# Optimization experiments

Measured on AMD Instinct MI355X. Metric: run time of the kernel, lower is better.

Reference implementation:

```python
import jax, jax.numpy as jnp
import numpy as np

N_NODES = 50000
N_EDGES = 300000
N_ETYPES = 4
D = 256          # input_dim == output_dim (no zero-pad branch in GatedGraphConv)
RES = 768        # res_feature_dim
N_GRAPHS = 128
N_STEPS = 8
HID = 256        # classifier hidden dim


def setup_inputs() -> dict:
    key = jax.random.key(0)
    ks = jax.random.split(key, 12)
    s = 0.05
    return {
        "features": jax.random.normal(ks[0], (N_NODES, D + RES), jnp.float32),
        "W_e": jax.random.normal(ks[1], (N_ETYPES, D, D), jnp.float32) * s,
        "b_e": jnp.zeros((N_ETYPES, D), jnp.float32),
        "W_ih": jax.random.normal(ks[2], (D, 3 * D), jnp.float32) * s,
        "W_hh": jax.random.normal(ks[3], (D, 3 * D), jnp.float32) * s,
        "b_ih": jnp.zeros((3 * D,), jnp.float32),
        "b_hh": jnp.zeros((3 * D,), jnp.float32),
        "W1": jax.random.normal(ks[4], (D + RES, HID), jnp.float32) * s,
        "b1": jnp.zeros((HID,), jnp.float32),
        "W2": jax.random.normal(ks[5], (HID, 1), jnp.float32) * s,
        "b2": jnp.zeros((1,), jnp.float32),
        "src": jax.random.randint(ks[6], (N_EDGES,), 0, N_NODES),
        "dst": jax.random.randint(ks[7], (N_EDGES,), 0, N_NODES),
        "etypes": jax.random.randint(ks[8], (N_EDGES,), 0, N_ETYPES),
        "node2graph": jnp.sort(jax.random.randint(ks[9], (N_NODES,), 0, N_GRAPHS)),
    }


def _gru_cell(x, h, W_ih, W_hh, b_ih, b_hh):
    # PyTorch GRUCell, gate order (r, z, n)
    gi = x @ W_ih + b_ih
    gh = h @ W_hh + b_hh
    i_r, i_z, i_n = jnp.split(gi, 3, axis=-1)
    h_r, h_z, h_n = jnp.split(gh, 3, axis=-1)
    r = jax.nn.sigmoid(i_r + h_r)
    z = jax.nn.sigmoid(i_z + h_z)
    n = jnp.tanh(i_n + r * h_n)
    return (1.0 - z) * n + z * h


def reference(features, W_e, b_e, W_ih, W_hh, b_ih, b_hh, W1, b1, W2, b2,
              src, dst, etypes, node2graph):
    h = features[:, :D]          # node features fed to GGNN
    res = features[:, D:]        # mixed residual features (bypass GGNN)

    def step(h, _):
        # per-edge-type linear on all nodes: [T, N, D]
        ht = jnp.einsum('nd,tde->tne', h, W_e) + b_e[:, None, :]
        msgs = ht[etypes, src]                                   # [E, D]
        a = jax.ops.segment_sum(msgs, dst, num_segments=N_NODES)  # scatter-add to dst
        return _gru_cell(a, h, W_ih, W_hh, b_ih, b_hh), None

    h, _ = jax.lax.scan(step, h, None, length=N_STEPS)

    out = jnp.concatenate([h, res], axis=1)  # [N, D+RES]
    # masked mean over nodes of each graph == segment mean
    sums = jax.ops.segment_sum(out, node2graph, num_segments=N_GRAPHS)
    cnts = jax.ops.segment_sum(jnp.ones((N_NODES,), out.dtype), node2graph,
                               num_segments=N_GRAPHS)
    pooled = sums / jnp.maximum(cnts, 1.0)[:, None]  # [B, D+RES]

    # classifier (dropouts inactive at eval): Linear -> ReLU -> Linear -> sigmoid
    hcls = jax.nn.relu(pooled @ W1 + b1)
    logits = hcls @ W2 + b2
    return jax.nn.sigmoid(logits)  # [B, 1]
```

## Files before the change

### kernel.cpp

```cpp
#include <hip/hip_runtime.h>
#include <math.h>
#include <stdint.h>

#define NN 50000
#define NE 300000
#define NT4 200000
#define NG 128
#define NSTEP 8
#define MPAD 50048
#define SCB 196
#define SCB2 782
#define PCH 8
#define EM 64
#define ECAP 896

typedef __attribute__((ext_vector_type(8))) short bf16x8;
typedef __attribute__((ext_vector_type(8))) unsigned short u16x8;
typedef __attribute__((ext_vector_type(4))) float f32x4;
typedef unsigned short u16;
typedef unsigned int u32;

__device__ __forceinline__ float b2f(u16 u) {
  union { u32 i; float f; } c; c.i = ((u32)u) << 16; return c.f;
}
__device__ __forceinline__ u16 f2b(float f) {
  union { float f; u32 i; } c; c.f = f;
  u32 x = c.i;
  u32 r = (x + 0x7fffu + ((x >> 16) & 1u)) >> 16;
  return (u16)r;
}

__device__ __forceinline__ void load_lds16(const void* g, void* l) {
  __builtin_amdgcn_global_load_lds((const __attribute__((address_space(1))) u32*)g,
                                   (__attribute__((address_space(3))) u32*)l, 16, 0, 0);
}

__global__ void k_conv_we(const float* __restrict__ W_e, u16* __restrict__ Wt) {
  int i = blockIdx.x * 256 + threadIdx.x;
  int c = i >> 8, d = i & 255;
  Wt[c * 256 + d] = f2b(W_e[(c >> 8) * 65536 + d * 256 + (c & 255)]);
}
__global__ void k_conv_rz(const float* __restrict__ W_ih, const float* __restrict__ W_hh,
                          u16* __restrict__ ah, u16* __restrict__ ha) {
  int i = blockIdx.x * 256 + threadIdx.x;
  int n = i >> 9, k = i & 511;
  float va = (k < 256) ? W_ih[k * 768 + n] : W_hh[(k - 256) * 768 + n];
  float vh = (k < 256) ? W_hh[k * 768 + n] : W_ih[(k - 256) * 768 + n];
  ah[n * 512 + k] = f2b(va);
  ha[n * 512 + k] = f2b(vh);
}
__global__ void k_conv_n(const float* __restrict__ W, u16* __restrict__ Wt) {
  int i = blockIdx.x * 256 + threadIdx.x;
  int n = i >> 8, k = i & 255;
  Wt[n * 256 + k] = f2b(W[k * 768 + 512 + n]);
}
__global__ void k_brz(const float* __restrict__ b_ih, const float* __restrict__ b_hh,
                      float* __restrict__ b_rz) {
  int i = blockIdx.x * 256 + threadIdx.x;
  if (i < 512) b_rz[i] = b_ih[i] + b_hh[i];
}

__global__ void k_init_h(const float* __restrict__ feat, u16* __restrict__ acat) {
  int i = blockIdx.x * 256 + threadIdx.x;
  int n = i >> 6, d = (i & 63) << 2;
  ushort4 o;
  if (n < NN) {
    float4 v = *(const float4*)(feat + (size_t)n * 1024 + d);
    o.x = f2b(v.x); o.y = f2b(v.y); o.z = f2b(v.z); o.w = f2b(v.w);
  } else {
    o.x = o.y = o.z = o.w = 0;
  }
  *(ushort4*)(acat + (size_t)n * 768 + d) = o;
}

__global__ void k_hist(const int* __restrict__ dst, const int* __restrict__ ety,
                       int* __restrict__ deg2) {
  int e = blockIdx.x * 256 + threadIdx.x;
  if (e < NE) atomicAdd(&deg2[dst[e] * 4 + ety[e]], 1);
}
__global__ void k_scan1(const int* __restrict__ deg2, int* __restrict__ part, int* __restrict__ bsum) {
  __shared__ int sh[256];
  int b = blockIdx.x, t = threadIdx.x;
  int i = b * 256 + t;
  int v = (i < NT4) ? deg2[i] : 0;
  sh[t] = v;
  __syncthreads();
  for (int off = 1; off < 256; off <<= 1) {
    int tmp = (t >= off) ? sh[t - off] : 0;
    __syncthreads();
    sh[t] += tmp;
    __syncthreads();
  }
  if (i < NT4) part[i] = sh[t] - v;
  if (t == 255) bsum[b] = sh[255];
}
__global__ void k_scan2(const int* __restrict__ bsum, int* __restrict__ boff) {
  __shared__ int sh[1024];
  int t = threadIdx.x;
  int v = (t < SCB2) ? bsum[t] : 0;
  sh[t] = v;
  __syncthreads();
  for (int off = 1; off < 1024; off <<= 1) {
    int tmp = (t >= off) ? sh[t - off] : 0;
    __syncthreads();
    sh[t] += tmp;
    __syncthreads();
  }
  boff[t] = sh[t] - v;
  if (t == 1023) boff[1024] = sh[1023];
}
__global__ void k_scan3(const int* __restrict__ part, const int* __restrict__ boff, int* __restrict__ rp2) {
  int i = blockIdx.x * 256 + threadIdx.x;
  if (i < NT4) rp2[i] = part[i] + boff[i >> 8];
  if (i == NT4) rp2[NT4] = boff[1024];
}
__global__ void k_scatter(const int* __restrict__ src, const int* __restrict__ dst,
                          const int* __restrict__ ety, const int* __restrict__ rp2,
                          int* __restrict__ cursor2, int* __restrict__ esrc) {
  int e = blockIdx.x * 256 + threadIdx.x;
  if (e < NE) {
    int seg = dst[e] * 4 + ety[e];
    int p = rp2[seg] + atomicAdd(&cursor2[seg], 1);
    esrc[p] = src[e];
  }
}
__global__ void k_cnt2(const int* __restrict__ deg2, ushort4* __restrict__ cnt2) {
  int v = blockIdx.x * 256 + threadIdx.x;
  if (v >= MPAD) return;
  ushort4 o;
  if (v < NN) {
    o.x = (u16)deg2[v * 4 + 0]; o.y = (u16)deg2[v * 4 + 1];
    o.z = (u16)deg2[v * 4 + 2]; o.w = (u16)deg2[v * 4 + 3];
  } else {
    o.x = o.y = o.z = o.w = 0;
  }
  cnt2[v] = o;
}
__global__ void k_gstart(const int* __restrict__ n2g, int* __restrict__ gstart) {
  int n = blockIdx.x * 256 + threadIdx.x;
  if (n >= NN) return;
  int g = n2g[n];
  int gp = (n == 0) ? -1 : n2g[n - 1];
  for (int x = gp + 1; x <= g; ++x) gstart[x] = n;
  if (n == NN - 1)
    for (int x = g + 1; x <= NG; ++x) gstart[x] = NN;
}

__global__ __launch_bounds__(512, 4) void k_eagg(
    const u16* __restrict__ acat, int hboff,
    const int* __restrict__ rp2, const int* __restrict__ esrc,
    const u16* __restrict__ Wt_e, const u16* __restrict__ Wt_in,
    const ushort4* __restrict__ cnt2, const float* __restrict__ b_e,
    const float* __restrict__ b_ih512,
    u16* __restrict__ acat_out, u16* __restrict__ inb) {
  __shared__ __align__(16) char Ss[EM * 512];
  __shared__ __align__(16) char BsB[2][16384];
  __shared__ int Es[ECAP];
  __shared__ int Rp[257];
  const int tid = threadIdx.x;
  const int wv = tid >> 6, l = tid & 63;
  const int hw = tid >> 5, lw = tid & 31;
  const int m0 = blockIdx.x * EM;
  const int fr = l & 15, kq = l >> 4;
  const int wm = (wv >> 2) * 32, wn = (wv & 3) * 64;

  const int base4 = m0 * 4;
  const int e0 = rp2[base4];
  for (int i = tid; i <= 256; i += 512) {
    int idx = base4 + i;
    if (idx > NT4) idx = NT4;
    Rp[i] = rp2[idx] - e0;
  }
  {
    int idxe = base4 + 256;
    if (idxe > NT4) idxe = NT4;
    int ecnt = rp2[idxe] - e0;
    int ecl = ecnt < ECAP ? ecnt : ECAP;
    for (int i = tid; i < ecl; i += 512) Es[i] = esrc[e0 + i] * 768 + hboff;
  }

  auto stageB = [&](int buf, int c) {
    const u16* W = (c < 32) ? (Wt_e + ((size_t)(c >> 3) << 16)) : Wt_in;
    int kbase = (c & 7) << 5;
#pragma unroll
    for (int p = 0; p < 2; ++p) {
      int i = p * 512 + tid;
      int row = i >> 2, slot = i & 3;
      load_lds16(W + (size_t)row * 256 + kbase + ((slot ^ ((row >> 1) & 3)) << 3),
                 BsB[buf] + p * 8192 + wv * 1024);
    }
  };

  __syncthreads();
  stageB(0, 0);

  f32x4 acc[2][4];
#pragma unroll
  for (int m = 0; m < 2; ++m)
#pragma unroll
    for (int n = 0; n < 4; ++n) acc[m][n] = (f32x4){0.f, 0.f, 0.f, 0.f};

  for (int t = 0; t < 4; ++t) {
    int cc[4], ee[4];
#pragma unroll
    for (int rr = 0; rr < 4; ++rr) {
      int li = (hw * 4 + rr) * 4 + t;
      cc[rr] = Rp[li];
      ee[rr] = Rp[li + 1];
    }
    float ar[4][8];
#pragma unroll
    for (int rr = 0; rr < 4; ++rr)
#pragma unroll
      for (int q = 0; q < 8; ++q) ar[rr][q] = 0.f;
    bool more = (cc[0] < ee[0]) | (cc[1] < ee[1]) | (cc[2] < ee[2]) | (cc[3] < ee[3]);
    while (more) {
      u16x8 v[4];
      bool p[4];
#pragma unroll
      for (int rr = 0; rr < 4; ++rr) {
        p[rr] = cc[rr] < ee[rr];
        if (p[rr]) {
          int rel = cc[rr];
          int off = (rel < ECAP) ? Es[rel] : (esrc[e0 + rel] * 768 + hboff);
          v[rr] = *(const u16x8*)(acat + (size_t)off + lw * 8);
        }
      }
#pragma unroll
      for (int rr = 0; rr < 4; ++rr) {
        if (p[rr]) {
#pragma unroll
          for (int q = 0; q < 8; ++q) ar[rr][q] += b2f(v[rr][q]);
          cc[rr]++;
        }
      }
      more = (cc[0] < ee[0]) | (cc[1] < ee[1]) | (cc[2] < ee[2]) | (cc[3] < ee[3]);
    }
#pragma unroll
    for (int rr = 0; rr < 4; ++rr) {
      int row = hw * 4 + rr;
      u16x8 o;
#pragma unroll
      for (int q = 0; q < 8; ++q) o[q] = f2b(ar[rr][q]);
      *(u16x8*)(Ss + row * 512 + ((lw * 16) ^ ((row & 7) << 4))) = o;
    }
    asm volatile("s_waitcnt lgkmcnt(0)" ::: "memory");
    __builtin_amdgcn_sched_barrier(0);

    for (int kc = 0; kc < 8; ++kc) {
      const int c = t * 8 + kc;
      const int buf = c & 1;
      stageB(buf ^ 1, c + 1);
      asm volatile("s_waitcnt vmcnt(2)" ::: "memory");
      __builtin_amdgcn_s_barrier();
      __builtin_amdgcn_sched_barrier(0);
      const char* BsC = BsB[buf];
      const int ka2 = (kc << 6) + (kq << 4);
      bf16x8 af[2], bfr[4];
#pragma unroll
      for (int m = 0; m < 2; ++m) {
        int R = wm + m * 16 + fr;
        af[m] = *(const bf16x8*)(Ss + R * 512 + (ka2 ^ ((R & 7) << 4)));
      }
#pragma unroll
      for (int n = 0; n < 4; ++n) {
        int R = wn + n * 16 + fr;
        bfr[n] = *(const bf16x8*)(BsC + R * 64 + ((kq ^ ((R >> 1) & 3)) << 4));
      }
#pragma unroll
      for (int m = 0; m < 2; ++m)
#pragma unroll
        for (int n = 0; n < 4; ++n)
          acc[m][n] = __builtin_amdgcn_mfma_f32_16x16x32_bf16(af[m], bfr[n], acc[m][n], 0, 0, 0);
      asm volatile("s_waitcnt lgkmcnt(0)" ::: "memory");
      __builtin_amdgcn_sched_barrier(0);
      __builtin_amdgcn_s_barrier();
    }
  }

  float bev[4][4];
#pragma unroll
  for (int n = 0; n < 4; ++n)
#pragma unroll
    for (int t = 0; t < 4; ++t) bev[n][t] = b_e[t * 256 + wn + n * 16 + fr];
#pragma unroll
  for (int m = 0; m < 2; ++m) {
#pragma unroll
    for (int j = 0; j < 4; ++j) {
      int r = wm + m * 16 + kq * 4 + j;
      int v = m0 + r;
      ushort4 c4 = cnt2[v];
      float c0 = c4.x, c1 = c4.y, c2 = c4.z, c3 = c4.w;
#pragma unroll
      for (int n = 0; n < 4; ++n) {
        int col = wn + n * 16 + fr;
        float val = acc[m][n][j] + c0 * bev[n][0] + c1 * bev[n][1] + c2 * bev[n][2] + c3 * bev[n][3];
        u16 vb = f2b(val);
        acat_out[(size_t)v * 768 + 256 + col] = vb;
        *(u16*)(Ss + r * 512 + ((col * 2) ^ ((r & 7) << 4))) = vb;
      }
    }
  }
#pragma unroll
  for (int m = 0; m < 2; ++m)
#pragma unroll
    for (int n = 0; n < 4; ++n) acc[m][n] = (f32x4){0.f, 0.f, 0.f, 0.f};
  asm volatile("s_waitcnt lgkmcnt(0)" ::: "memory");
  __builtin_amdgcn_sched_barrier(0);

  for (int kc = 0; kc < 8; ++kc) {
    const int c = 32 + kc;
    const int buf = c & 1;
    if (kc < 7) {
      stageB(buf ^ 1, c + 1);
      asm volatile("s_waitcnt vmcnt(2)" ::: "memory");
    } else {
      asm volatile("s_waitcnt vmcnt(0)" ::: "memory");
    }
    __builtin_amdgcn_s_barrier();
    __builtin_amdgcn_sched_barrier(0);
    const char* BsC = BsB[buf];
    const int ka2 = (kc << 6) + (kq << 4);
    bf16x8 af[2], bfr[4];
#pragma unroll
    for (int m = 0; m < 2; ++m) {
      int R = wm + m * 16 + fr;
      af[m] = *(const bf16x8*)(Ss + R * 512 + (ka2 ^ ((R & 7) << 4)));
    }
#pragma unroll
    for (int n = 0; n < 4; ++n) {
      int R = wn + n * 16 + fr;
      bfr[n] = *(const bf16x8*)(BsC + R * 64 + ((kq ^ ((R >> 1) & 3)) << 4));
    }
#pragma unroll
    for (int m = 0; m < 2; ++m)
#pragma unroll
      for (int n = 0; n < 4; ++n)
        acc[m][n] = __builtin_amdgcn_mfma_f32_16x16x32_bf16(af[m], bfr[n], acc[m][n], 0, 0, 0);
    asm volatile("s_waitcnt lgkmcnt(0)" ::: "memory");
    __builtin_amdgcn_sched_barrier(0);
    __builtin_amdgcn_s_barrier();
  }

  float bi[4];
#pragma unroll
  for (int n = 0; n < 4; ++n) bi[n] = b_ih512[wn + n * 16 + fr];
#pragma unroll
  for (int m = 0; m < 2; ++m) {
#pragma unroll
    for (int j = 0; j < 4; ++j) {
      int v = m0 + wm + m * 16 + kq * 4 + j;
#pragma unroll
      for (int n = 0; n < 4; ++n) {
        int col = wn + n * 16 + fr;
        inb[(size_t)v * 256 + col] = f2b(acc[m][n][j] + bi[n]);
      }
    }
  }
}

template <int MODE>
__global__ __launch_bounds__(512, 2) void k_gemm2(
    const u16* __restrict__ A, int lda, int K,
    const u16* __restrict__ Bt, const float* __restrict__ bias,
    u16* __restrict__ C, int ldc,
    const u16* __restrict__ rzb, const u16* __restrict__ inb,
    const u16* __restrict__ hold, u16* __restrict__ hnew) {
  __shared__ __align__(16) char AsB[2][64 * 128];
  __shared__ __align__(16) char BsB[2][256 * 128];
  const int tid = threadIdx.x;
  const int wv = tid >> 6, l = tid & 63;
  const int m0 = blockIdx.y * 64, n0 = blockIdx.x * 256;
  const int fr = l & 15, kq = l >> 4;
  const int wm = (wv >> 2) * 32, wn = (wv & 3) * 64;
  const int arow = tid >> 3, acl = tid & 7;

  f32x4 acc[2][4];
#pragma unroll
  for (int m = 0; m < 2; ++m)
#pragma unroll
    for (int n = 0; n < 4; ++n) acc[m][n] = (f32x4){0.f, 0.f, 0.f, 0.f};

  auto stage = [&](int buf, int k0) {
    load_lds16(A + (size_t)(m0 + arow) * lda + k0 + ((acl ^ (arow & 7)) << 3),
               AsB[buf] + wv * 1024);
#pragma unroll
    for (int p = 0; p < 4; ++p) {
      int brow = p * 64 + arow;
      load_lds16(Bt + (size_t)(n0 + brow) * K + k0 + ((acl ^ (brow & 7)) << 3),
                 BsB[buf] + p * 8192 + wv * 1024);
    }
  };

  stage(0, 0);
  const int NK = K >> 6;
  for (int ki = 0; ki < NK; ++ki) {
    const int cur = ki & 1;
    if (ki + 1 < NK) {
      stage(cur ^ 1, (ki + 1) << 6);
      asm volatile("s_waitcnt vmcnt(5)" ::: "memory");
    } else {
      asm volatile("s_waitcnt vmcnt(0)" ::: "memory");
    }
    __builtin_amdgcn_s_barrier();
    __builtin_amdgcn_sched_barrier(0);
    const char* As = AsB[cur];
    const char* Bs = BsB[cur];
#pragma unroll
    for (int kk = 0; kk < 64; kk += 32) {
      bf16x8 af[2], bfr[4];
      int kb = (kk + kq * 8) * 2;
#pragma unroll
      for (int m = 0; m < 2; ++m) {
        int R = wm + m * 16 + fr;
        af[m] = *(const bf16x8*)(As + R * 128 + (kb ^ ((R & 7) << 4)));
      }
#pragma unroll
      for (int n = 0; n < 4; ++n) {
        int R = wn + n * 16 + fr;
        bfr[n] = *(const bf16x8*)(Bs + R * 128 + (kb ^ ((R & 7) << 4)));
      }
#pragma unroll
      for (int m = 0; m < 2; ++m)
#pragma unroll
        for (int n = 0; n < 4; ++n)
          acc[m][n] = __builtin_amdgcn_mfma_f32_16x16x32_bf16(af[m], bfr[n], acc[m][n], 0, 0, 0);
    }
    asm volatile("s_waitcnt lgkmcnt(0)" ::: "memory");
    __builtin_amdgcn_sched_barrier(0);
    __builtin_amdgcn_s_barrier();
  }

#pragma unroll
  for (int m = 0; m < 2; ++m) {
#pragma unroll
    for (int j = 0; j < 4; ++j) {
      int row = m0 + wm + m * 16 + kq * 4 + j;
#pragma unroll
      for (int n = 0; n < 4; ++n) {
        int col = n0 + wn + n * 16 + fr;
        float v = acc[m][n][j] + bias[col];
        if (MODE == 1) {
          C[(size_t)row * ldc + col] = f2b(1.f / (1.f + expf(-v)));
        } else {
          float r = b2f(rzb[(size_t)row * 512 + col]);
          float z = b2f(rzb[(size_t)row * 512 + 256 + col]);
          float in_ = b2f(inb[(size_t)row * 256 + col]);
          float ho = b2f(hold[(size_t)row * 768 + col]);
          float ng = tanhf(in_ + r * v);
          hnew[(size_t)row * 768 + col] = f2b((1.f - z) * ng + z * ho);
        }
      }
    }
  }
}

__global__ __launch_bounds__(256) void k_pool(const u16* __restrict__ hb, const float* __restrict__ feat,
                                              const int* __restrict__ gstart, float* __restrict__ pooled) {
  int g = blockIdx.x, ch = blockIdx.y, t = threadIdx.x;
  int s = gstart[g], e = gstart[g + 1];
  int tot = e - s;
  int per = (tot + PCH - 1) / PCH;
  int ns = s + ch * per;
  int ne = ns + per < e ? ns + per : e;
  if (ns >= ne) return;
  int c = t << 2;
  float a0 = 0.f, a1 = 0.f, a2 = 0.f, a3 = 0.f;
  if (c < 256) {
    for (int n = ns; n < ne; ++n) {
      ushort4 u = *(const ushort4*)(hb + (size_t)n * 768 + c);
      a0 += b2f(u.x); a1 += b2f(u.y); a2 += b2f(u.z); a3 += b2f(u.w);
    }
  } else {
    for (int n = ns; n < ne; ++n) {
      float4 v = *(const float4*)(feat + (size_t)n * 1024 + c);
      a0 += v.x; a1 += v.y; a2 += v.z; a3 += v.w;
    }
  }
  atomicAdd(&pooled[g * 1024 + c], a0);
  atomicAdd(&pooled[g * 1024 + c + 1], a1);
  atomicAdd(&pooled[g * 1024 + c + 2], a2);
  atomicAdd(&pooled[g * 1024 + c + 3], a3);
}

__global__ __launch_bounds__(256) void k_head(const float* __restrict__ pooled,
                                              const int* __restrict__ gstart,
                                              const float* __restrict__ W1, const float* __restrict__ b1,
                                              const float* __restrict__ W2, const float* __restrict__ b2,
                                              float* __restrict__ out) {
  __shared__ float sp[1024];
  __shared__ float red[256];
  int g = blockIdx.x, t = threadIdx.x;
  float inv = 1.f / fmaxf((float)(gstart[g + 1] - gstart[g]), 1.f);
  for (int i = t; i < 1024; i += 256) sp[i] = pooled[g * 1024 + i] * inv;
  __syncthreads();
  float acc = b1[t];
  for (int k = 0; k < 1024; ++k) acc += sp[k] * W1[k * 256 + t];
  float hc = fmaxf(acc, 0.f);
  red[t] = hc * W2[t];
  __syncthreads();
  for (int s2 = 128; s2 > 0; s2 >>= 1) {
    if (t < s2) red[t] += red[t + s2];
    __syncthreads();
  }
  if (t == 0) out[g] = 1.f / (1.f + expf(-(red[0] + b2[0])));
}

extern "C" void kernel_launch(void* const* d_in, const int* in_sizes, int n_in, void* d_out, int out_size,
                              void* d_ws, size_t ws_size, hipStream_t stream) {
  const float* feat = (const float*)d_in[0];
  const float* W_e = (const float*)d_in[1];
  const float* b_e = (const float*)d_in[2];
  const float* W_ih = (const float*)d_in[3];
  const float* W_hh = (const float*)d_in[4];
  const float* b_ih = (const float*)d_in[5];
  const float* b_hh = (const float*)d_in[6];
  const float* W1 = (const float*)d_in[7];
  const float* b1 = (const float*)d_in[8];
  const float* W2 = (const float*)d_in[9];
  const float* b2 = (const float*)d_in[10];
  const int* src = (const int*)d_in[11];
  const int* dst = (const int*)d_in[12];
  const int* ety = (const int*)d_in[13];
  const int* n2g = (const int*)d_in[14];

  char* p = (char*)d_ws;
  auto alloc = [&](size_t b) { char* r = p; p += (b + 255) & ~(size_t)255; return r; };
  u16* acat = (u16*)alloc((size_t)MPAD * 768 * 2);
  u16* rzb = (u16*)alloc((size_t)MPAD * 512 * 2);
  u16* inb = (u16*)alloc((size_t)MPAD * 256 * 2);
  u16* Wt_e = (u16*)alloc(1024 * 256 * 2);
  u16* Wt_rz_ah = (u16*)alloc(512 * 512 * 2);
  u16* Wt_rz_ha = (u16*)alloc(512 * 512 * 2);
  u16* Wt_in = (u16*)alloc(256 * 256 * 2);
  u16* Wt_hn = (u16*)alloc(256 * 256 * 2);
  float* b_rz = (float*)alloc(512 * 4);
  int* deg2 = (int*)alloc((size_t)NT4 * 4);
  int* part = (int*)alloc((size_t)NT4 * 4);
  int* bsum = (int*)alloc((size_t)SCB2 * 4);
  int* boff = (int*)alloc(1025 * 4);
  int* rp2 = (int*)alloc((size_t)(NT4 + 1) * 4);
  int* cursor2 = (int*)alloc((size_t)NT4 * 4);
  int* esrc = (int*)alloc((size_t)NE * 4);
  ushort4* cnt2 = (ushort4*)alloc((size_t)MPAD * 8);
  int* gstart = (int*)alloc((size_t)(NG + 1) * 4);
  float* pooled = (float*)alloc((size_t)NG * 1024 * 4);

  hipMemsetAsync(deg2, 0, (size_t)NT4 * 4, stream);
  hipMemsetAsync(cursor2, 0, (size_t)NT4 * 4, stream);
  hipMemsetAsync(pooled, 0, (size_t)NG * 1024 * 4, stream);

  k_conv_we<<<1024, 256, 0, stream>>>(W_e, Wt_e);
  k_conv_rz<<<1024, 256, 0, stream>>>(W_ih, W_hh, Wt_rz_ah, Wt_rz_ha);
  k_conv_n<<<256, 256, 0, stream>>>(W_ih, Wt_in);
  k_conv_n<<<256, 256, 0, stream>>>(W_hh, Wt_hn);
  k_brz<<<2, 256, 0, stream>>>(b_ih, b_hh, b_rz);
  k_init_h<<<MPAD / 4, 256, 0, stream>>>(feat, acat);
  k_hist<<<(NE + 255) / 256, 256, 0, stream>>>(dst, ety, deg2);
  k_scan1<<<SCB2, 256, 0, stream>>>(deg2, part, bsum);
  k_scan2<<<1, 1024, 0, stream>>>(bsum, boff);
  k_scan3<<<SCB2 + 1, 256, 0, stream>>>(part, boff, rp2);
  k_scatter<<<(NE + 255) / 256, 256, 0, stream>>>(src, dst, ety, rp2, cursor2, esrc);
  k_cnt2<<<(MPAD + 255) / 256, 256, 0, stream>>>(deg2, cnt2);
  k_gstart<<<SCB, 256, 0, stream>>>(n2g, gstart);

  const int GY = MPAD / 64;
  for (int s = 0; s < NSTEP; ++s) {
    int hboff = (s & 1) ? 512 : 0;
    int hnewoff = 512 - hboff;
    int rzoff = (s & 1) ? 256 : 0;
    const u16* Wrz = (s & 1) ? Wt_rz_ah : Wt_rz_ha;
    k_eagg<<<MPAD / EM, 512, 0, stream>>>(acat, hboff, rp2, esrc, Wt_e, Wt_in, cnt2, b_e,
                                          b_ih + 512, acat, inb);
    k_gemm2<1><<<dim3(2, GY), 512, 0, stream>>>(acat + rzoff, 768, 512, Wrz, b_rz, rzb, 512,
                                                nullptr, nullptr, nullptr, nullptr);
    k_gemm2<2><<<dim3(1, GY), 512, 0, stream>>>(acat + hboff, 768, 256, Wt_hn, b_hh + 512,
                                                nullptr, 0, rzb, inb, acat + hboff,
                                                acat + hnewoff);
  }

  k_pool<<<dim3(NG, PCH), 256, 0, stream>>>(acat, feat, gstart, pooled);
  k_head<<<NG, 256, 0, stream>>>(pooled, gstart, W1, b1, W2, b2, (float*)d_out);
}
```

Before: 1.673 ms.

## Single-buffer weight tiles and shrink edge cache to raise eagg occupancy

Drops double buffering of the weight tile in LDS and shrinks the cached edge-source array, cutting shared memory per block. The gather loop now handles two rows at a time instead of four to lower register pressure. Launch bounds ask for 6 blocks per CU instead of 4. The trade is that weight loads are no longer overlapped with MFMA work, since each chunk waits on vmcnt(0). The smaller gather batch also gives fewer loads in flight per wave, and more edges take the slower global fallback path.

```diff
diff --git a/kernel.cpp b/kernel.cpp
--- a/kernel.cpp
+++ b/kernel.cpp
@@ -12,7 +12,7 @@
 #define SCB2 782
 #define PCH 8
 #define EM 64
-#define ECAP 896
+#define ECAP 640
 
 typedef __attribute__((ext_vector_type(8))) short bf16x8;
 typedef __attribute__((ext_vector_type(8))) unsigned short u16x8;
@@ -146,7 +146,7 @@
     for (int x = g + 1; x <= NG; ++x) gstart[x] = NN;
 }
 
-__global__ __launch_bounds__(512, 4) void k_eagg(
+__global__ __launch_bounds__(512, 6) void k_eagg(
     const u16* __restrict__ acat, int hboff,
     const int* __restrict__ rp2, const int* __restrict__ esrc,
     const u16* __restrict__ Wt_e, const u16* __restrict__ Wt_in,
@@ -154,7 +154,7 @@
     const float* __restrict__ b_ih512,
     u16* __restrict__ acat_out, u16* __restrict__ inb) {
   __shared__ __align__(16) char Ss[EM * 512];
-  __shared__ __align__(16) char BsB[2][16384];
+  __shared__ __align__(16) char Bs[16384];
   __shared__ int Es[ECAP];
   __shared__ int Rp[257];
   const int tid = threadIdx.x;
@@ -178,8 +178,9 @@
     int ecl = ecnt < ECAP ? ecnt : ECAP;
     for (int i = tid; i < ecl; i += 512) Es[i] = esrc[e0 + i] * 768 + hboff;
   }
-
-  auto stageB = [&](int buf, int c) {
+  __syncthreads();
+
+  auto stageB = [&](int c) {
     const u16* W = (c < 32) ? (Wt_e + ((size_t)(c >> 3) << 16)) : Wt_in;
     int kbase = (c & 7) << 5;
 #pragma unroll
@@ -187,13 +188,10 @@
       int i = p * 512 + tid;
       int row = i >> 2, slot = i & 3;
       load_lds16(W + (size_t)row * 256 + kbase + ((slot ^ ((row >> 1) & 3)) << 3),
-                 BsB[buf] + p * 8192 + wv * 1024);
+                 Bs + p * 8192 + wv * 1024);
     }
   };
 
-  __syncthreads();
-  stageB(0, 0);
-
   f32x4 acc[2][4];
 #pragma unroll
   for (int m = 0; m < 2; ++m)
@@ -201,60 +199,60 @@
     for (int n = 0; n < 4; ++n) acc[m][n] = (f32x4){0.f, 0.f, 0.f, 0.f};
 
   for (int t = 0; t < 4; ++t) {
-    int cc[4], ee[4];
-#pragma unroll
-    for (int rr = 0; rr < 4; ++rr) {
-      int li = (hw * 4 + rr) * 4 + t;
-      cc[rr] = Rp[li];
-      ee[rr] = Rp[li + 1];
-    }
-    float ar[4][8];
-#pragma unroll
-    for (int rr = 0; rr < 4; ++rr)
-#pragma unroll
-      for (int q = 0; q < 8; ++q) ar[rr][q] = 0.f;
-    bool more = (cc[0] < ee[0]) | (cc[1] < ee[1]) | (cc[2] < ee[2]) | (cc[3] < ee[3]);
-    while (more) {
-      u16x8 v[4];
-      bool p[4];
-#pragma unroll
-      for (int rr = 0; rr < 4; ++rr) {
-        p[rr] = cc[rr] < ee[rr];
-        if (p[rr]) {
-          int rel = cc[rr];
-          int off = (rel < ECAP) ? Es[rel] : (esrc[e0 + rel] * 768 + hboff);
-          v[rr] = *(const u16x8*)(acat + (size_t)off + lw * 8);
+#pragma unroll
+    for (int g2 = 0; g2 < 2; ++g2) {
+      int cc[2], ee[2];
+#pragma unroll
+      for (int rr = 0; rr < 2; ++rr) {
+        int li = (hw * 4 + g2 * 2 + rr) * 4 + t;
+        cc[rr] = Rp[li];
+        ee[rr] = Rp[li + 1];
+      }
+      float ar[2][8];
+#pragma unroll
+      for (int rr = 0; rr < 2; ++rr)
+#pragma unroll
+        for (int q = 0; q < 8; ++q) ar[rr][q] = 0.f;
+      bool more = (cc[0] < ee[0]) | (cc[1] < ee[1]);
+      while (more) {
+        u16x8 v[2];
+        bool p[2];
+#pragma unroll
+        for (int rr = 0; rr < 2; ++rr) {
+          p[rr] = cc[rr] < ee[rr];
+          if (p[rr]) {
+            int rel = cc[rr];
+            int off = (rel < ECAP) ? Es[rel] : (esrc[e0 + rel] * 768 + hboff);
+            v[rr] = *(const u16x8*)(acat + (size_t)off + lw * 8);
+          }
         }
-      }
-#pragma unroll
-      for (int rr = 0; rr < 4; ++rr) {
-        if (p[rr]) {
-#pragma unroll
-          for (int q = 0; q < 8; ++q) ar[rr][q] += b2f(v[rr][q]);
-          cc[rr]++;
+#pragma unroll
+        for (int rr = 0; rr < 2; ++rr) {
+          if (p[rr]) {
+#pragma unroll
+            for (int q = 0; q < 8; ++q) ar[rr][q] += b2f(v[rr][q]);
+            cc[rr]++;
+          }
         }
-      }
-      more = (cc[0] < ee[0]) | (cc[1] < ee[1]) | (cc[2] < ee[2]) | (cc[3] < ee[3]);
-    }
-#pragma unroll
-    for (int rr = 0; rr < 4; ++rr) {
-      int row = hw * 4 + rr;
-      u16x8 o;
-#pragma unroll
-      for (int q = 0; q < 8; ++q) o[q] = f2b(ar[rr][q]);
-      *(u16x8*)(Ss + row * 512 + ((lw * 16) ^ ((row & 7) << 4))) = o;
+        more = (cc[0] < ee[0]) | (cc[1] < ee[1]);
+      }
+#pragma unroll
+      for (int rr = 0; rr < 2; ++rr) {
+        int row = hw * 4 + g2 * 2 + rr;
+        u16x8 o;
+#pragma unroll
+        for (int q = 0; q < 8; ++q) o[q] = f2b(ar[rr][q]);
+        *(u16x8*)(Ss + row * 512 + ((lw * 16) ^ ((row & 7) << 4))) = o;
+      }
     }
     asm volatile("s_waitcnt lgkmcnt(0)" ::: "memory");
     __builtin_amdgcn_sched_barrier(0);
 
     for (int kc = 0; kc < 8; ++kc) {
-      const int c = t * 8 + kc;
-      const int buf = c & 1;
-      stageB(buf ^ 1, c + 1);
-      asm volatile("s_waitcnt vmcnt(2)" ::: "memory");
+      stageB(t * 8 + kc);
+      asm volatile("s_waitcnt vmcnt(0)" ::: "memory");
       __builtin_amdgcn_s_barrier();
       __builtin_amdgcn_sched_barrier(0);
-      const char* BsC = BsB[buf];
       const int ka2 = (kc << 6) + (kq << 4);
       bf16x8 af[2], bfr[4];
 #pragma unroll
@@ -265,7 +263,7 @@
 #pragma unroll
       for (int n = 0; n < 4; ++n) {
         int R = wn + n * 16 + fr;
-        bfr[n] = *(const bf16x8*)(BsC + R * 64 + ((kq ^ ((R >> 1) & 3)) << 4));
+        bfr[n] = *(const bf16x8*)(Bs + R * 64 + ((kq ^ ((R >> 1) & 3)) << 4));
       }
 #pragma unroll
       for (int m = 0; m < 2; ++m)
@@ -309,17 +307,10 @@
   __builtin_amdgcn_sched_barrier(0);
 
   for (int kc = 0; kc < 8; ++kc) {
-    const int c = 32 + kc;
-    const int buf = c & 1;
-    if (kc < 7) {
-      stageB(buf ^ 1, c + 1);
-      asm volatile("s_waitcnt vmcnt(2)" ::: "memory");
-    } else {
-      asm volatile("s_waitcnt vmcnt(0)" ::: "memory");
-    }
+    stageB(32 + kc);
+    asm volatile("s_waitcnt vmcnt(0)" ::: "memory");
     __builtin_amdgcn_s_barrier();
     __builtin_amdgcn_sched_barrier(0);
-    const char* BsC = BsB[buf];
     const int ka2 = (kc << 6) + (kq << 4);
     bf16x8 af[2], bfr[4];
 #pragma unroll
@@ -330,7 +321,7 @@
 #pragma unroll
     for (int n = 0; n < 4; ++n) {
       int R = wn + n * 16 + fr;
-      bfr[n] = *(const bf16x8*)(BsC + R * 64 + ((kq ^ ((R >> 1) & 3)) << 4));
+      bfr[n] = *(const bf16x8*)(Bs + R * 64 + ((kq ^ ((R >> 1) & 3)) << 4));
     }
 #pragma unroll
     for (int m = 0; m < 2; ++m)
```

Result: slower. 1.944 ms (+16.2%).
